# Optimization experiments

Hardware: AMD Instinct MI355X
Metric: run time of the kernel (lower is better)

## Reference

```python
import jax, jax.numpy as jnp
import numpy as np

N, E = 100000, 1600000
IN_CH, HID, HEADS, OUT_CH = 128, 32, 2, 40
NEG_SLOPE = 0.2
BN_EPS = 1e-5


def _param(key, shape, scale=0.1):
    return scale * jax.random.normal(key, shape, dtype=jnp.float32)


def setup_inputs() -> dict:
    key = jax.random.key(0)
    ks = jax.random.split(key, 24)
    x = jax.random.normal(ks[0], (N, IN_CH), dtype=jnp.float32)
    edge_index = jax.random.randint(ks[1], (2, E), 0, N, dtype=jnp.int32)
    d0 = HEADS * HID  # 64
    inp = {
        'x': x, 'edge_index': edge_index,
        # conv0: in 128 -> 32 per head, concat -> 64
        'W0': _param(ks[2], (IN_CH, HEADS * HID)),
        'as0': _param(ks[3], (HEADS, HID)), 'ad0': _param(ks[4], (HEADS, HID)),
        'b0': jnp.zeros((d0,), jnp.float32),
        'g0': jnp.ones((d0,), jnp.float32), 'bt0': jnp.zeros((d0,), jnp.float32),
        # conv1: 64 -> 32 per head, concat -> 64
        'W1': _param(ks[5], (d0, HEADS * HID)),
        'as1': _param(ks[6], (HEADS, HID)), 'ad1': _param(ks[7], (HEADS, HID)),
        'b1': jnp.zeros((d0,), jnp.float32),
        'g1': jnp.ones((d0,), jnp.float32), 'bt1': jnp.zeros((d0,), jnp.float32),
        # conv2: 64 -> 40 per head, mean over heads -> 40
        'W2': _param(ks[8], (d0, HEADS * OUT_CH)),
        'as2': _param(ks[9], (HEADS, OUT_CH)), 'ad2': _param(ks[10], (HEADS, OUT_CH)),
        'b2': jnp.zeros((OUT_CH,), jnp.float32),
    }
    return inp


def gat_conv(x, src, dst, W, a_src, a_dst, bias, out_ch, concat):
    n = x.shape[0]
    h = (x @ W).reshape(n, HEADS, out_ch)            # [N,H,C]
    alpha_src = jnp.sum(h * a_src, axis=-1)          # [N,H]
    alpha_dst = jnp.sum(h * a_dst, axis=-1)          # [N,H]
    e = jax.nn.leaky_relu(alpha_src[src] + alpha_dst[dst], NEG_SLOPE)  # [E,H]
    # softmax over incoming edges per destination node (self loops guarantee >=1 edge)
    m = jax.ops.segment_max(e, dst, num_segments=n)
    e = jnp.exp(e - m[dst])
    s = jax.ops.segment_sum(e, dst, num_segments=n)
    alpha = e / s[dst]                                # [E,H]
    msg = h[src] * alpha[:, :, None]                  # [E,H,C]
    out = jax.ops.segment_sum(msg, dst, num_segments=n)  # [N,H,C]
    out = out.reshape(n, HEADS * out_ch) if concat else out.mean(axis=1)
    return out + bias


def batch_norm(x, gamma, beta):
    mu = jnp.mean(x, axis=0)
    var = jnp.mean(jnp.square(x - mu), axis=0)
    return gamma * (x - mu) * jax.lax.rsqrt(var + BN_EPS) + beta


def reference(x, edge_index, W0, as0, ad0, b0, g0, bt0,
              W1, as1, ad1, b1, g1, bt1, W2, as2, ad2, b2):
    n = x.shape[0]
    loops = jnp.arange(n, dtype=edge_index.dtype)
    src = jnp.concatenate([edge_index[0], loops])
    dst = jnp.concatenate([edge_index[1], loops])
    h = gat_conv(x, src, dst, W0, as0, ad0, b0, HID, True)
    h = jax.nn.elu(batch_norm(h, g0, bt0))
    h = gat_conv(h, src, dst, W1, as1, ad1, b1, HID, True)
    h = jax.nn.elu(batch_norm(h, g1, bt1))
    return gat_conv(h, src, dst, W2, as2, ad2, b2, OUT_CH, False)
```

## Files before the change

kernel.cpp:

```cpp
#include <hip/hip_runtime.h>
#include <hip/hip_bf16.h>
#include <math.h>


#define NNODES 100000
#define NEDGES 1600000
#define ENTOT  (NEDGES + NNODES)
#define NEG_SLOPE 0.2f
#define BN_EPS 1e-5f

#define NRANGE 8
#define RSIZE  (NNODES/NRANGE)
#define BCAP   262144
#define PBLK   2048
#define NB2    32

typedef unsigned short u16;
typedef unsigned int u32;
typedef unsigned long long u64;
typedef __attribute__((ext_vector_type(8))) short short8;
typedef __attribute__((ext_vector_type(4))) float f32x4;

__device__ __forceinline__ float b2f(u16 u){ union{u32 i; float f;} v; v.i=((u32)u)<<16; return v.f; }
__device__ __forceinline__ float blo(u32 u){ union{u32 i; float f;} v; v.i=u<<16; return v.f; }
__device__ __forceinline__ float bhi(u32 u){ union{u32 i; float f;} v; v.i=u&0xffff0000u; return v.f; }
__device__ __forceinline__ u16 f2b(float x){ __hip_bfloat16 b=__float2bfloat16(x); return *(u16*)&b; }
__device__ __forceinline__ float ldf(const void* p, int i, int f){
  return f ? ((const float*)p)[i] : b2f(((const u16*)p)[i]);
}

__global__ void k_detect(const u16* __restrict__ x, int* __restrict__ flag){
  __shared__ int bad;
  if(threadIdx.x==0) bad=0;
  __syncthreads();
  int cnt=0;
  for(int i=threadIdx.x;i<4096;i+=256){
    u16 v = x[2*i];
    int ex = (v>>7)&0xff;
    if(ex==0xff || (ex==0 && (v&0x7fff)!=0)) cnt++;
  }
  atomicAdd(&bad,cnt);
  __syncthreads();
  if(threadIdx.x==0) flag[0] = (bad>4)?1:0;
}

__global__ __launch_bounds__(256) void k_part2(
    const int* __restrict__ ei, int* __restrict__ gptr, u32* __restrict__ bkt){
  __shared__ int lcnt[NRANGE], gbase[NRANGE];
  int t=threadIdx.x;
  if(t<NRANGE) lcnt[t]=0;
  __syncthreads();
  const int CH=(ENTOT+PBLK-1)/PBLK;
  int beg=blockIdx.x*CH, end=beg+CH; if(end>ENTOT) end=ENTOT;
  int nd[4], ns[4], nr[4], ne=0;
  for(int i=beg+t; i<end; i+=256){
    int d=(i<NEDGES)? ei[NEDGES+i] : (i-NEDGES);
    int s=(i<NEDGES)? ei[i] : d;
    nd[ne]=d; ns[ne]=s; ne++;
  }
  #pragma unroll 4
  for(int k=0;k<ne;k++) nr[k]=atomicAdd(&lcnt[nd[k]/RSIZE],1);
  __syncthreads();
  if(t<NRANGE) gbase[t]=atomicAdd(&gptr[t],lcnt[t]);
  __syncthreads();
  #pragma unroll 4
  for(int k=0;k<ne;k++){
    int r=nd[k]/RSIZE;
    u32 e = ((u32)(nd[k]-r*RSIZE)<<17) | (u32)ns[k];
    __builtin_nontemporal_store(e, &bkt[(size_t)r*BCAP + gbase[r] + nr[k]]);
  }
}

__global__ __launch_bounds__(256) void k_hist4(
    const u32* __restrict__ bkt, const int* __restrict__ gptr, int* __restrict__ lhist){
  __shared__ int lh[RSIZE];
  int t=threadIdx.x;
  for(int i=t;i<RSIZE;i+=256) lh[i]=0;
  __syncthreads();
  int r = blockIdx.x & (NRANGE-1);
  int c = blockIdx.x >> 3;
  int n = gptr[r];
  int per=(n+NB2-1)/NB2;
  int beg=c*per, end=beg+per; if(end>n) end=n;
  const u32* bp = bkt + (size_t)r*BCAP;
  for(int i=beg+t;i<end;i+=256) atomicAdd(&lh[bp[i]>>17],1);
  __syncthreads();
  int* out = lhist + (size_t)(r*NB2+c)*RSIZE;
  for(int i=t;i<RSIZE;i+=256) out[i]=lh[i];
}

__global__ __launch_bounds__(256) void k_sumscan(int* __restrict__ lhist, int* __restrict__ cnt){
  int n = blockIdx.x*256 + threadIdx.x;
  if(n>=NNODES) return;
  int r = n/RSIZE, i = n - r*RSIZE;
  int* base = lhist + (size_t)r*NB2*RSIZE + i;
  int run=0;
  #pragma unroll 8
  for(int c=0;c<NB2;c++){
    int v = base[(size_t)c*RSIZE];
    base[(size_t)c*RSIZE] = run;
    run += v;
  }
  cnt[n]=run;
}

#define SCAN_M (NNODES+1)
#define SCAN_NB ((SCAN_M + 2047)/2048)

__global__ void k_scan_a(const int* __restrict__ cnt, int* __restrict__ bsum){
  __shared__ int red[256];
  int b=blockIdx.x, t=threadIdx.x;
  int base = b*2048 + t*8;
  int s=0;
  #pragma unroll
  for(int j=0;j<8;j++){ int idx=base+j; s += (idx<NNODES)? cnt[idx]:0; }
  red[t]=s; __syncthreads();
  for(int o=128;o>0;o>>=1){ if(t<o) red[t]+=red[t+o]; __syncthreads(); }
  if(t==0) bsum[b]=red[0];
}

__global__ void k_scan_b(int* bsum){
  if(threadIdx.x==0){
    int run=0;
    for(int i=0;i<SCAN_NB;i++){ int v=bsum[i]; bsum[i]=run; run+=v; }
  }
}

__global__ void k_scan_c(const int* __restrict__ cnt, const int* __restrict__ bsum,
                         int* __restrict__ row_ptr){
  __shared__ int lds[256];
  int b=blockIdx.x, t=threadIdx.x;
  int base=b*2048+t*8;
  int v[8]; int s=0;
  #pragma unroll
  for(int j=0;j<8;j++){ int idx=base+j; int x=(idx<NNODES)?cnt[idx]:0; v[j]=s; s+=x; }
  lds[t]=s; __syncthreads();
  for(int o=1;o<256;o<<=1){
    int other=0; if(t>=o) other=lds[t-o];
    __syncthreads();
    lds[t]+=other;
    __syncthreads();
  }
  int texcl = lds[t] - s;
  int off0 = bsum[b] + texcl;
  #pragma unroll
  for(int j=0;j<8;j++){ int idx=base+j; if(idx<SCAN_M) row_ptr[idx]=off0+v[j]; }
}

__global__ __launch_bounds__(256) void k_scatter4(
    const u32* __restrict__ bkt, const int* __restrict__ gptr,
    const int* __restrict__ row_ptr, const int* __restrict__ lhist,
    int* __restrict__ col){
  __shared__ int lofs[RSIZE];
  int t=threadIdx.x;
  int r = blockIdx.x & (NRANGE-1);
  int c = blockIdx.x >> 3;
  int lo = r*RSIZE;
  const int* cb = lhist + (size_t)(r*NB2+c)*RSIZE;
  for(int i=t;i<RSIZE;i+=256) lofs[i] = row_ptr[lo+i] + cb[i];
  __syncthreads();
  int n = gptr[r];
  int per=(n+NB2-1)/NB2;
  int beg=c*per, end=beg+per; if(end>n) end=n;
  const u32* bp = bkt + (size_t)r*BCAP;
  for(int i=beg+t;i<end;i+=256){
    u32 e=bp[i];
    int pos=atomicAdd(&lofs[e>>17],1);
    col[pos]=(int)(e & 0x1FFFF);
  }
}

__global__ __launch_bounds__(256) void k_binsort(
    const int* __restrict__ row_ptr, const int* __restrict__ col,
    int* __restrict__ col2){
  int d = blockIdx.x*256 + threadIdx.x;
  if(d>=NNODES) return;
  int b0=row_ptr[d], b1=row_ptr[d+1];
  u64 cntp=0;
  for(int j=b0;j<b1;j++){
    int sb = col[j]/RSIZE;
    cntp += 1ull << (sb*8);
  }
  u64 offp=0; u32 run=0;
  #pragma unroll
  for(int sb=0;sb<8;sb++){
    offp |= (u64)(run&0xffu) << (sb*8);
    run += (u32)((cntp >> (sb*8)) & 0xff);
  }
  for(int j=b0;j<b1;j++){
    int c = col[j];
    int sb = c/RSIZE;
    int pos = b0 + (int)((offp>>(sb*8))&0xff);
    offp += 1ull << (sb*8);
    col2[pos]=c;
  }
}

template<int K, int OUTC, int HID, bool XEXT, bool BN>
__global__ __launch_bounds__(256) void k_gemm_mfma(
    const void* __restrict__ xin, const void* __restrict__ W,
    const void* __restrict__ avs, const void* __restrict__ avd,
    const float2* __restrict__ bnab,
    u16* __restrict__ hout, float* __restrict__ asrc, float* __restrict__ adst,
    const int* __restrict__ flagp)
{
  const int f = flagp[0];
  constexpr int KP = K+8;
  constexpr int RS = OUTC+8;
  constexpr int NT = OUTC/16;
  constexpr int KQ = K/32;
  __shared__ __align__(16) u16 WT[OUTC*KP];
  __shared__ __align__(16) u16 HROW[4*16*RS];
  __shared__ float AVb[2*OUTC];
  __shared__ float2 BB[K];
  int t=threadIdx.x;
  const u16* Wu=(const u16*)W; const float* Wf=(const float*)W;
  for(int i8=t*8; i8<K*OUTC; i8+=256*8){
    int k=i8/OUTC, c0=i8-k*OUTC;
    u16 w8[8];
    if(f){
      const float* wp=Wf+i8;
      float4 a=*(const float4*)wp, b=*(const float4*)(wp+4);
      w8[0]=f2b(a.x);w8[1]=f2b(a.y);w8[2]=f2b(a.z);w8[3]=f2b(a.w);
      w8[4]=f2b(b.x);w8[5]=f2b(b.y);w8[6]=f2b(b.z);w8[7]=f2b(b.w);
    } else {
      uint4 q=*(const uint4*)(Wu+i8);
      w8[0]=q.x&0xffff;w8[1]=q.x>>16;w8[2]=q.y&0xffff;w8[3]=q.y>>16;
      w8[4]=q.z&0xffff;w8[5]=q.z>>16;w8[6]=q.w&0xffff;w8[7]=q.w>>16;
    }
    #pragma unroll
    for(int u=0;u<8;u++) WT[(c0+u)*KP + k] = w8[u];
  }
  for(int idx=t; idx<2*OUTC; idx+=256)
    AVb[idx] = (idx<OUTC)? ldf(avs,idx,f) : ldf(avd,idx-OUTC,f);
  if(BN) for(int idx=t; idx<K; idx+=256) BB[idx]=bnab[idx];
  __syncthreads();

  int wv=t>>6, lane=t&63;
  int m=lane&15, quad=lane>>4;
  int grow0 = blockIdx.x*64 + wv*16;
  int growA = grow0 + m;
  bool avalid = growA < NNODES;
  int growC = avalid ? growA : 0;

  f32x4 acc[NT] = {};
  #pragma unroll
  for(int kq=0;kq<KQ;kq++){
    int k0 = kq*32 + quad*8;
    union{ u32 u[4]; short8 s8; } A;
    if(XEXT && f==1){
      const float* xr=(const float*)xin + (size_t)growC*K + k0;
      float4 p=*(const float4*)xr, q=*(const float4*)(xr+4);
      A.u[0]=f2b(p.x)|((u32)f2b(p.y)<<16);
      A.u[1]=f2b(p.z)|((u32)f2b(p.w)<<16);
      A.u[2]=f2b(q.x)|((u32)f2b(q.y)<<16);
      A.u[3]=f2b(q.z)|((u32)f2b(q.w)<<16);
    } else {
      uint4 q=*(const uint4*)((const u16*)xin + (size_t)growC*K + k0);
      A.u[0]=q.x; A.u[1]=q.y; A.u[2]=q.z; A.u[3]=q.w;
    }
    if(BN){
      #pragma unroll
      for(int j=0;j<4;j++){
        float lo=b2f(A.u[j]&0xffff), hi=b2f(A.u[j]>>16);
        float2 c1=BB[k0+2*j], c2=BB[k0+2*j+1];
        lo=c1.x*lo+c1.y; lo = lo>0.f? lo : __expf(lo)-1.f;
        hi=c2.x*hi+c2.y; hi = hi>0.f? hi : __expf(hi)-1.f;
        A.u[j]=f2b(lo)|((u32)f2b(hi)<<16);
      }
    }
    #pragma unroll
    for(int nt=0;nt<NT;nt++){
      union{ uint4 q; short8 s8; } Bf;
      Bf.q = *(const uint4*)&WT[(nt*16+m)*KP + k0];
      acc[nt] = __builtin_amdgcn_mfma_f32_16x16x32_bf16(A.s8, Bf.s8, acc[nt], 0,0,0);
    }
  }
  u16* hr = &HROW[wv*16*RS];
  #pragma unroll
  for(int nt=0;nt<NT;nt++){
    #pragma unroll
    for(int reg=0;reg<4;reg++)
      hr[(quad*4+reg)*RS + nt*16+m] = f2b(acc[nt][reg]);
  }
  __syncthreads();
  {
    int row=lane&15, task=quad, head=task&1, sd=task>>1;
    float p=0.f;
    const u16* hrow=&hr[row*RS + head*HID];
    const float* av=&AVb[sd*OUTC + head*HID];
    #pragma unroll 8
    for(int c=0;c<HID;c++) p += b2f(hrow[c])*av[c];
    int grow=grow0+row;
    if(grow<NNODES){ (sd? adst:asrc)[grow*2+head]=p; }
  }
  {
    constexpr int CH8 = OUTC/8;
    for(int idx=lane; idx<16*CH8; idx+=64){
      int rr=idx/CH8, c8=idx-rr*CH8;
      int grow=grow0+rr;
      if(grow<NNODES)
        *(uint4*)(hout + (size_t)grow*OUTC + c8*8) = *(const uint4*)&hr[rr*RS + c8*8];
    }
  }
}

template<int OUTC, bool FINAL>
__global__ __launch_bounds__(256) void k_aggf(
  const int* __restrict__ row_ptr, const int* __restrict__ col2,
  const u16* __restrict__ hin, const float2* __restrict__ asrc2,
  const float2* __restrict__ adst2, const void* __restrict__ bias,
  u16* __restrict__ houtb, void* __restrict__ outv, const int* __restrict__ flagp)
{
  const int f = flagp[0];
  __shared__ float vbuf[FINAL?32:1][84];
  constexpr int HSPLIT = FINAL ? 5 : 4;
  int t = threadIdx.x;
  int g  = t>>3;
  int cg = t&7;
  int rr = blockIdx.x & 7, jb = blockIdx.x >> 3;
  int lim = RSIZE - jb*32;
  bool ok = g < lim;
  int d = rr*RSIZE + jb*32 + g;
  int base=0, deg=0;
  float2 adv = make_float2(0.f,0.f);
  if(ok){
    base = row_ptr[d];
    deg  = row_ptr[d+1] - base;
    adv  = adst2[d];
  }
  const int* cp  = col2 + base;
  const u16* hcg = hin + cg*8;
  const u16* hxg = hin + 64 + cg*2;
  float acc[8]={0,0,0,0,0,0,0,0}, accx0=0.f, accx1=0.f;
  float s0=0.f, s1=0.f;

  for(int ph=0; ph<8; ++ph){
    int beg = (deg*ph)>>3;
    int end = (deg*(ph+1))>>3;
    for(int j=beg; j<end; j+=2){
      int c0 = cp[j];
      bool v1 = (j+1)<end;
      int c1 = cp[v1 ? j+1 : j];
      float2 sa = asrc2[c0];
      float2 sv = asrc2[c1];
      const u16* hp0 = hcg + (size_t)c0*OUTC;
      const u16* hp1 = hcg + (size_t)c1*OUTC;
      uint4 h0 = *(const uint4*)hp0;
      uint4 h1 = *(const uint4*)hp1;
      float e0 = sa.x+adv.x; e0 = fmaxf(e0, NEG_SLOPE*e0); e0 = fminf(e0,60.f);
      float e1 = sa.y+adv.y; e1 = fmaxf(e1, NEG_SLOPE*e1); e1 = fminf(e1,60.f);
      float p0 = __expf(e0), p1 = __expf(e1);
      float q0 = sv.x+adv.x; q0 = fmaxf(q0, NEG_SLOPE*q0); q0 = fminf(q0,60.f);
      float q1 = sv.y+adv.y; q1 = fmaxf(q1, NEG_SLOPE*q1); q1 = fminf(q1,60.f);
      float r0 = __expf(q0), r1 = __expf(q1);
      if(!v1){ r0=0.f; r1=0.f; }
      s0 += p0 + r0; s1 += p1 + r1;
      float pa = (cg<HSPLIT)? p0 : p1;
      float pb = (cg<HSPLIT)? r0 : r1;
      acc[0] += pa*blo(h0.x) + pb*blo(h1.x);
      acc[1] += pa*bhi(h0.x) + pb*bhi(h1.x);
      acc[2] += pa*blo(h0.y) + pb*blo(h1.y);
      acc[3] += pa*bhi(h0.y) + pb*bhi(h1.y);
      acc[4] += pa*blo(h0.z) + pb*blo(h1.z);
      acc[5] += pa*bhi(h0.z) + pb*bhi(h1.z);
      acc[6] += pa*blo(h0.w) + pb*blo(h1.w);
      acc[7] += pa*bhi(h0.w) + pb*bhi(h1.w);
      if(FINAL){
        ushort2 ha = *(const ushort2*)(hxg + (size_t)c0*OUTC);
        ushort2 hb = *(const ushort2*)(hxg + (size_t)c1*OUTC);
        accx0 += p1*b2f(ha.x) + r1*b2f(hb.x);
        accx1 += p1*b2f(ha.y) + r1*b2f(hb.y);
      }
    }
    __syncthreads();
  }

  float inv0 = s0>0.f?1.f/s0:0.f, inv1 = s1>0.f?1.f/s1:0.f;
  if(!FINAL){
    if(ok){
      float inv = (cg<4)? inv0 : inv1;
      u16 o8[8];
      #pragma unroll
      for(int k=0;k<8;k++) o8[k]=f2b(acc[k]*inv + ldf(bias,cg*8+k,f));
      uint4 ov;
      ov.x=(u32)o8[0]|((u32)o8[1]<<16); ov.y=(u32)o8[2]|((u32)o8[3]<<16);
      ov.z=(u32)o8[4]|((u32)o8[5]<<16); ov.w=(u32)o8[6]|((u32)o8[7]<<16);
      *(uint4*)(houtb + (size_t)d*64 + cg*8) = ov;
    }
  } else {
    if(ok){
      #pragma unroll
      for(int k=0;k<8;k++)
        vbuf[g][cg*8+k] = acc[k]*((cg<5)?inv0:inv1);
      vbuf[g][64+cg*2]   = accx0*inv1;
      vbuf[g][64+cg*2+1] = accx1*inv1;
    }
    __syncthreads();
    for(int idx=t; idx<32*40; idx+=256){
      int gg=idx/40, ch=idx-gg*40;
      if(gg<lim){
        int dd = rr*RSIZE + jb*32 + gg;
        float res = 0.5f*(vbuf[gg][ch] + vbuf[gg][40+ch]) + ldf(bias,ch,f);
        if(f) ((float*)outv)[(size_t)dd*40+ch] = res;
        else  ((__hip_bfloat16*)outv)[(size_t)dd*40+ch] = __float2bfloat16(res);
      }
    }
  }
}

__global__ __launch_bounds__(256) void k_bnstats(const u16* __restrict__ h, float* __restrict__ stats){
  __shared__ float red[4][128];
  int t=threadIdx.x; int c=t&63; int g=t>>6;
  float s=0.f,q=0.f;
  for(int r=blockIdx.x*4+g; r<NNODES; r+=gridDim.x*4){
    float v=b2f(h[(size_t)r*64+c]); s+=v; q+=v*v;
  }
  red[g][c]=s; red[g][64+c]=q;
  __syncthreads();
  if(t<128){
    float tot=red[0][t]+red[1][t]+red[2][t]+red[3][t];
    atomicAdd(&stats[t], tot);
  }
}

__global__ void k_bnfinal(const float* __restrict__ stats,
                          const void* __restrict__ gm, const void* __restrict__ bt,
                          float2* __restrict__ bnab, const int* __restrict__ flagp){
  const int f = flagp[0];
  int c=threadIdx.x;
  if(c>=64) return;
  float mu=stats[c]*(1.0f/NNODES);
  float var=stats[64+c]*(1.0f/NNODES)-mu*mu;
  var = var>0.f?var:0.f;
  float A = ldf(gm,c,f)*rsqrtf(var+BN_EPS);
  float B = ldf(bt,c,f) - A*mu;
  bnab[c]=make_float2(A,B);
}

extern "C" void kernel_launch(void* const* d_in, const int* in_sizes, int n_in,
                              void* d_out, int out_size, void* d_ws, size_t ws_size,
                              hipStream_t stream){
  const void* x  =d_in[0];
  const int* ei =(const int*)d_in[1];
  const void* W0 =d_in[2];  const void* as0=d_in[3];  const void* ad0=d_in[4];
  const void* b0 =d_in[5];  const void* g0 =d_in[6];  const void* bt0=d_in[7];
  const void* W1 =d_in[8];  const void* as1=d_in[9];  const void* ad1=d_in[10];
  const void* b1 =d_in[11]; const void* g1 =d_in[12]; const void* bt1=d_in[13];
  const void* W2 =d_in[14]; const void* as2=d_in[15]; const void* ad2=d_in[16];
  const void* b2 =d_in[17];

  char* ws=(char*)d_ws;
  size_t off=0;
  auto alloc=[&](size_t bytes)->void*{ void* p=ws+off; off+=(bytes+255)&~(size_t)255; return p; };
  int*    flag   =(int*)   alloc(256);
  int*    row_ptr=(int*)   alloc((size_t)(NNODES+1)*4);
  int*    cnt    =(int*)   alloc((size_t)NNODES*4);
  int*    colx   =(int*)   alloc((size_t)ENTOT*4);
  int*    colx2  =(int*)   alloc((size_t)ENTOT*4);
  int*    bsum   =(int*)   alloc((size_t)SCAN_NB*4);
  int*    gptr   =(int*)   alloc(256);
  u32*    bkt    =(u32*)   alloc((size_t)NRANGE*BCAP*4);
  u16*    hA     =(u16*)   alloc((size_t)100032*80*2);
  u16*    hB0    =(u16*)   alloc((size_t)100032*64*2);
  u16*    hB1    =(u16*)   alloc((size_t)100032*64*2);
  float*  asrc   =(float*) alloc((size_t)NNODES*2*4);
  float*  adst   =(float*) alloc((size_t)NNODES*2*4);
  float*  stats  =(float*) alloc(128*4);
  float2* bnab   =(float2*)alloc(64*8);
  int*    lhist  =(int*)hA;

  k_detect<<<1,256,0,stream>>>((const u16*)x, flag);

  (void)hipMemsetAsync(gptr,0,256,stream);
  k_part2  <<<PBLK,256,0,stream>>>(ei,gptr,bkt);
  k_hist4  <<<NRANGE*NB2,256,0,stream>>>(bkt,gptr,lhist);
  k_sumscan<<<(NNODES+255)/256,256,0,stream>>>(lhist,cnt);
  k_scan_a <<<SCAN_NB,256,0,stream>>>(cnt,bsum);
  k_scan_b <<<1,64,0,stream>>>(bsum);
  k_scan_c <<<SCAN_NB,256,0,stream>>>(cnt,bsum,row_ptr);
  k_scatter4<<<NRANGE*NB2,256,0,stream>>>(bkt,gptr,row_ptr,lhist,colx);
  k_binsort<<<(NNODES+255)/256,256,0,stream>>>(row_ptr,colx,colx2);

  int gG = (NNODES+63)/64;
  int gA = NRANGE * ((RSIZE + 31)/32);
  k_gemm_mfma<128,64,32,true ,false><<<gG,256,0,stream>>>(
      x,W0,as0,ad0,nullptr,hA,asrc,adst,flag);
  k_aggf<64,false><<<gA,256,0,stream>>>(row_ptr,colx2,hA,
      (const float2*)asrc,(const float2*)adst,b0,hB0,nullptr,flag);
  (void)hipMemsetAsync(stats,0,512,stream);
  k_bnstats<<<256,256,0,stream>>>(hB0,stats);
  k_bnfinal<<<1,64,0,stream>>>(stats,g0,bt0,bnab,flag);
  k_gemm_mfma<64,64,32,false,true ><<<gG,256,0,stream>>>(
      hB0,W1,as1,ad1,bnab,hA,asrc,adst,flag);
  k_aggf<64,false><<<gA,256,0,stream>>>(row_ptr,colx2,hA,
      (const float2*)asrc,(const float2*)adst,b1,hB1,nullptr,flag);
  (void)hipMemsetAsync(stats,0,512,stream);
  k_bnstats<<<256,256,0,stream>>>(hB1,stats);
  k_bnfinal<<<1,64,0,stream>>>(stats,g1,bt1,bnab,flag);
  k_gemm_mfma<64,80,40,false,true ><<<gG,256,0,stream>>>(
      hB1,W2,as2,ad2,bnab,hA,asrc,adst,flag);
  k_aggf<80,true ><<<gA,256,0,stream>>>(row_ptr,colx2,hA,
      (const float2*)asrc,(const float2*)adst,b2,nullptr,d_out,flag);

  (void)in_sizes;(void)n_in;(void)out_size;(void)ws_size;
}
```

Baseline: 472.7 us.

## Stage binsort columns in LDS, compute one head per thread, use fewer sync phases

k_binsort now loads each block's contiguous slice of column indices into shared memory, so the two passes over them read LDS instead of global memory. The 64-channel aggregation kernels compute only the attention score of the head each thread owns, which halves the exp work, and read a single float of asrc instead of a float2. Both aggregation variants split the edge loop into 4 block-synchronised phases instead of 8, trading locality pacing across threads for fewer barriers.

```diff
diff --git a/kernel.cpp b/kernel.cpp
--- a/kernel.cpp
+++ b/kernel.cpp
@@ -14,6 +14,7 @@
 #define BCAP   262144
 #define PBLK   2048
 #define NB2    32
+#define BSL    8192
 
 typedef unsigned short u16;
 typedef unsigned int u32;
@@ -173,26 +174,36 @@
 __global__ __launch_bounds__(256) void k_binsort(
     const int* __restrict__ row_ptr, const int* __restrict__ col,
     int* __restrict__ col2){
-  int d = blockIdx.x*256 + threadIdx.x;
-  if(d>=NNODES) return;
-  int b0=row_ptr[d], b1=row_ptr[d+1];
-  u64 cntp=0;
-  for(int j=b0;j<b1;j++){
-    int sb = col[j]/RSIZE;
-    cntp += 1ull << (sb*8);
-  }
-  u64 offp=0; u32 run=0;
-  #pragma unroll
-  for(int sb=0;sb<8;sb++){
-    offp |= (u64)(run&0xffu) << (sb*8);
-    run += (u32)((cntp >> (sb*8)) & 0xff);
-  }
-  for(int j=b0;j<b1;j++){
-    int c = col[j];
-    int sb = c/RSIZE;
-    int pos = b0 + (int)((offp>>(sb*8))&0xff);
-    offp += 1ull << (sb*8);
-    col2[pos]=c;
+  __shared__ int lcol[BSL];
+  int t = threadIdx.x;
+  int blk0 = blockIdx.x*256;
+  int d1 = blk0+256; if(d1>NNODES) d1=NNODES;
+  int s0 = row_ptr[blk0], s1 = row_ptr[d1];
+  int n = s1 - s0;
+  bool fit = (n<=BSL);
+  if(fit){ for(int i=t;i<n;i+=256) lcol[i]=col[s0+i]; }
+  __syncthreads();
+  int d = blk0 + t;
+  if(d<NNODES){
+    int b0=row_ptr[d], b1=row_ptr[d+1];
+    u64 cntp=0;
+    for(int j=b0;j<b1;j++){
+      int c = fit ? lcol[j-s0] : col[j];
+      cntp += 1ull << ((c/RSIZE)*8);
+    }
+    u64 offp=0; u32 run=0;
+    #pragma unroll
+    for(int sb=0;sb<8;sb++){
+      offp |= (u64)(run&0xffu) << (sb*8);
+      run += (u32)((cntp >> (sb*8)) & 0xff);
+    }
+    for(int j=b0;j<b1;j++){
+      int c = fit ? lcol[j-s0] : col[j];
+      int sb = c/RSIZE;
+      int pos = b0 + (int)((offp>>(sb*8))&0xff);
+      offp += 1ull << (sb*8);
+      col2[pos]=c;
+    }
   }
 }
 
@@ -308,13 +319,12 @@
 template<int OUTC, bool FINAL>
 __global__ __launch_bounds__(256) void k_aggf(
   const int* __restrict__ row_ptr, const int* __restrict__ col2,
-  const u16* __restrict__ hin, const float2* __restrict__ asrc2,
+  const u16* __restrict__ hin, const float* __restrict__ asrcf,
   const float2* __restrict__ adst2, const void* __restrict__ bias,
   u16* __restrict__ houtb, void* __restrict__ outv, const int* __restrict__ flagp)
 {
   const int f = flagp[0];
   __shared__ float vbuf[FINAL?32:1][84];
-  constexpr int HSPLIT = FINAL ? 5 : 4;
   int t = threadIdx.x;
   int g  = t>>3;
   int cg = t&7;
@@ -331,55 +341,41 @@
   }
   const int* cp  = col2 + base;
   const u16* hcg = hin + cg*8;
-  const u16* hxg = hin + 64 + cg*2;
-  float acc[8]={0,0,0,0,0,0,0,0}, accx0=0.f, accx1=0.f;
-  float s0=0.f, s1=0.f;
-
-  for(int ph=0; ph<8; ++ph){
-    int beg = (deg*ph)>>3;
-    int end = (deg*(ph+1))>>3;
-    for(int j=beg; j<end; j+=2){
-      int c0 = cp[j];
-      bool v1 = (j+1)<end;
-      int c1 = cp[v1 ? j+1 : j];
-      float2 sa = asrc2[c0];
-      float2 sv = asrc2[c1];
-      const u16* hp0 = hcg + (size_t)c0*OUTC;
-      const u16* hp1 = hcg + (size_t)c1*OUTC;
-      uint4 h0 = *(const uint4*)hp0;
-      uint4 h1 = *(const uint4*)hp1;
-      float e0 = sa.x+adv.x; e0 = fmaxf(e0, NEG_SLOPE*e0); e0 = fminf(e0,60.f);
-      float e1 = sa.y+adv.y; e1 = fmaxf(e1, NEG_SLOPE*e1); e1 = fminf(e1,60.f);
-      float p0 = __expf(e0), p1 = __expf(e1);
-      float q0 = sv.x+adv.x; q0 = fmaxf(q0, NEG_SLOPE*q0); q0 = fminf(q0,60.f);
-      float q1 = sv.y+adv.y; q1 = fmaxf(q1, NEG_SLOPE*q1); q1 = fminf(q1,60.f);
-      float r0 = __expf(q0), r1 = __expf(q1);
-      if(!v1){ r0=0.f; r1=0.f; }
-      s0 += p0 + r0; s1 += p1 + r1;
-      float pa = (cg<HSPLIT)? p0 : p1;
-      float pb = (cg<HSPLIT)? r0 : r1;
-      acc[0] += pa*blo(h0.x) + pb*blo(h1.x);
-      acc[1] += pa*bhi(h0.x) + pb*bhi(h1.x);
-      acc[2] += pa*blo(h0.y) + pb*blo(h1.y);
-      acc[3] += pa*bhi(h0.y) + pb*bhi(h1.y);
-      acc[4] += pa*blo(h0.z) + pb*blo(h1.z);
-      acc[5] += pa*bhi(h0.z) + pb*bhi(h1.z);
-      acc[6] += pa*blo(h0.w) + pb*blo(h1.w);
-      acc[7] += pa*bhi(h0.w) + pb*bhi(h1.w);
-      if(FINAL){
-        ushort2 ha = *(const ushort2*)(hxg + (size_t)c0*OUTC);
-        ushort2 hb = *(const ushort2*)(hxg + (size_t)c1*OUTC);
-        accx0 += p1*b2f(ha.x) + r1*b2f(hb.x);
-        accx1 += p1*b2f(ha.y) + r1*b2f(hb.y);
+  float acc[8]={0,0,0,0,0,0,0,0};
+
+  if(!FINAL){
+    int ho = (cg>=4)?1:0;
+    float aown = ho ? adv.y : adv.x;
+    float s=0.f;
+    for(int ph=0; ph<4; ++ph){
+      int beg = (deg*ph)>>2;
+      int end = (deg*(ph+1))>>2;
+      for(int j=beg; j<end; j+=2){
+        int c0 = cp[j];
+        bool v1 = (j+1)<end;
+        int c1 = cp[v1 ? j+1 : j];
+        float sa = asrcf[c0*2+ho];
+        float sb = asrcf[c1*2+ho];
+        uint4 h0 = *(const uint4*)(hcg + (size_t)c0*OUTC);
+        uint4 h1 = *(const uint4*)(hcg + (size_t)c1*OUTC);
+        float e0 = sa+aown; e0 = fmaxf(e0, NEG_SLOPE*e0); e0 = fminf(e0,60.f);
+        float e1 = sb+aown; e1 = fmaxf(e1, NEG_SLOPE*e1); e1 = fminf(e1,60.f);
+        float p0 = __expf(e0), p1 = __expf(e1);
+        if(!v1) p1 = 0.f;
+        s += p0 + p1;
+        acc[0] += p0*blo(h0.x) + p1*blo(h1.x);
+        acc[1] += p0*bhi(h0.x) + p1*bhi(h1.x);
+        acc[2] += p0*blo(h0.y) + p1*blo(h1.y);
+        acc[3] += p0*bhi(h0.y) + p1*bhi(h1.y);
+        acc[4] += p0*blo(h0.z) + p1*blo(h1.z);
+        acc[5] += p0*bhi(h0.z) + p1*bhi(h1.z);
+        acc[6] += p0*blo(h0.w) + p1*blo(h1.w);
+        acc[7] += p0*bhi(h0.w) + p1*bhi(h1.w);
       }
-    }
-    __syncthreads();
-  }
-
-  float inv0 = s0>0.f?1.f/s0:0.f, inv1 = s1>0.f?1.f/s1:0.f;
-  if(!FINAL){
+      __syncthreads();
+    }
+    float inv = s>0.f ? 1.f/s : 0.f;
     if(ok){
-      float inv = (cg<4)? inv0 : inv1;
       u16 o8[8];
       #pragma unroll
       for(int k=0;k<8;k++) o8[k]=f2b(acc[k]*inv + ldf(bias,cg*8+k,f));
@@ -389,6 +385,49 @@
       *(uint4*)(houtb + (size_t)d*64 + cg*8) = ov;
     }
   } else {
+    const float2* asrc2 = (const float2*)asrcf;
+    const u16* hxg = hin + 64 + cg*2;
+    float accx0=0.f, accx1=0.f;
+    float s0=0.f, s1=0.f;
+    for(int ph=0; ph<4; ++ph){
+      int beg = (deg*ph)>>2;
+      int end = (deg*(ph+1))>>2;
+      for(int j=beg; j<end; j+=2){
+        int c0 = cp[j];
+        bool v1 = (j+1)<end;
+        int c1 = cp[v1 ? j+1 : j];
+        float2 sa = asrc2[c0];
+        float2 sv = asrc2[c1];
+        const u16* hp0 = hcg + (size_t)c0*OUTC;
+        const u16* hp1 = hcg + (size_t)c1*OUTC;
+        uint4 h0 = *(const uint4*)hp0;
+        uint4 h1 = *(const uint4*)hp1;
+        float e0 = sa.x+adv.x; e0 = fmaxf(e0, NEG_SLOPE*e0); e0 = fminf(e0,60.f);
+        float e1 = sa.y+adv.y; e1 = fmaxf(e1, NEG_SLOPE*e1); e1 = fminf(e1,60.f);
+        float p0 = __expf(e0), p1 = __expf(e1);
+        float q0 = sv.x+adv.x; q0 = fmaxf(q0, NEG_SLOPE*q0); q0 = fminf(q0,60.f);
+        float q1 = sv.y+adv.y; q1 = fmaxf(q1, NEG_SLOPE*q1); q1 = fminf(q1,60.f);
+        float r0 = __expf(q0), r1 = __expf(q1);
+        if(!v1){ r0=0.f; r1=0.f; }
+        s0 += p0 + r0; s1 += p1 + r1;
+        float pa = (cg<5)? p0 : p1;
+        float pb = (cg<5)? r0 : r1;
+        acc[0] += pa*blo(h0.x) + pb*blo(h1.x);
+        acc[1] += pa*bhi(h0.x) + pb*bhi(h1.x);
+        acc[2] += pa*blo(h0.y) + pb*blo(h1.y);
+        acc[3] += pa*bhi(h0.y) + pb*bhi(h1.y);
+        acc[4] += pa*blo(h0.z) + pb*blo(h1.z);
+        acc[5] += pa*bhi(h0.z) + pb*bhi(h1.z);
+        acc[6] += pa*blo(h0.w) + pb*blo(h1.w);
+        acc[7] += pa*bhi(h0.w) + pb*bhi(h1.w);
+        ushort2 ha = *(const ushort2*)(hxg + (size_t)c0*OUTC);
+        ushort2 hb = *(const ushort2*)(hxg + (size_t)c1*OUTC);
+        accx0 += p1*b2f(ha.x) + r1*b2f(hb.x);
+        accx1 += p1*b2f(ha.y) + r1*b2f(hb.y);
+      }
+      __syncthreads();
+    }
+    float inv0 = s0>0.f?1.f/s0:0.f, inv1 = s1>0.f?1.f/s1:0.f;
     if(ok){
       #pragma unroll
       for(int k=0;k<8;k++)
@@ -487,21 +526,21 @@
   k_gemm_mfma<128,64,32,true ,false><<<gG,256,0,stream>>>(
       x,W0,as0,ad0,nullptr,hA,asrc,adst,flag);
   k_aggf<64,false><<<gA,256,0,stream>>>(row_ptr,colx2,hA,
-      (const float2*)asrc,(const float2*)adst,b0,hB0,nullptr,flag);
+      asrc,(const float2*)adst,b0,hB0,nullptr,flag);
   (void)hipMemsetAsync(stats,0,512,stream);
   k_bnstats<<<256,256,0,stream>>>(hB0,stats);
   k_bnfinal<<<1,64,0,stream>>>(stats,g0,bt0,bnab,flag);
   k_gemm_mfma<64,64,32,false,true ><<<gG,256,0,stream>>>(
       hB0,W1,as1,ad1,bnab,hA,asrc,adst,flag);
   k_aggf<64,false><<<gA,256,0,stream>>>(row_ptr,colx2,hA,
-      (const float2*)asrc,(const float2*)adst,b1,hB1,nullptr,flag);
+      asrc,(const float2*)adst,b1,hB1,nullptr,flag);
   (void)hipMemsetAsync(stats,0,512,stream);
   k_bnstats<<<256,256,0,stream>>>(hB1,stats);
   k_bnfinal<<<1,64,0,stream>>>(stats,g1,bt1,bnab,flag);
   k_gemm_mfma<64,80,40,false,true ><<<gG,256,0,stream>>>(
       hB1,W2,as2,ad2,bnab,hA,asrc,adst,flag);
   k_aggf<80,true ><<<gA,256,0,stream>>>(row_ptr,colx2,hA,
-      (const float2*)asrc,(const float2*)adst,b2,nullptr,d_out,flag);
+      asrc,(const float2*)adst,b2,nullptr,d_out,flag);
 
   (void)in_sizes;(void)n_in;(void)out_size;(void)ws_size;
 }
```

After: 466.1 us. Within noise of the previous version (-1.4%).
